# Kernel tuning notes

Measured on AMD Instinct MI355X. Metric: run time of the kernel, lower is better.

## Reference

```python
import jax, jax.numpy as jnp
import numpy as np

B, T, D_MODEL = 2, 2048, 2048
N_HEAD, N_KV = 16, 4
HEAD_DIM = D_MODEL // N_HEAD  # 128
N_REP = N_HEAD // N_KV        # 4
ROPE_BASE = 10000.0


def setup_inputs() -> dict:
    key = jax.random.key(0)
    ks = jax.random.split(key, 5)
    s = 0.02
    return {
        "x": jax.random.normal(ks[0], (B, T, D_MODEL), dtype=jnp.float32),
        "Wq": jax.random.normal(ks[1], (D_MODEL, N_HEAD * HEAD_DIM), dtype=jnp.float32) * s,
        "Wk": jax.random.normal(ks[2], (D_MODEL, N_KV * HEAD_DIM), dtype=jnp.float32) * s,
        "Wv": jax.random.normal(ks[3], (D_MODEL, N_KV * HEAD_DIM), dtype=jnp.float32) * s,
        "Wo": jax.random.normal(ks[4], (D_MODEL, D_MODEL), dtype=jnp.float32) * s,
    }


def _rope_cos_sin(seq_len, dim, dtype):
    inv_freq = 1.0 / (ROPE_BASE ** (jnp.arange(0, dim, 2, dtype=jnp.float32) / dim))
    t = jnp.arange(seq_len, dtype=jnp.float32)
    freqs = t[:, None] * inv_freq[None, :]          # (T, dim/2)
    emb = jnp.concatenate([freqs, freqs], axis=-1)  # (T, dim)
    return jnp.cos(emb).astype(dtype), jnp.sin(emb).astype(dtype)


def _rotate_half(x):
    half = x.shape[-1] // 2
    return jnp.concatenate([-x[..., half:], x[..., :half]], axis=-1)


def reference(x, Wq, Wk, Wv, Wo):
    Bx, Tx, _ = x.shape
    # projections (weights stored (in, out); equals torch Linear with W^T)
    q = (x @ Wq).reshape(Bx, Tx, N_HEAD, HEAD_DIM).transpose(0, 2, 1, 3)  # (B,H,T,d)
    k = (x @ Wk).reshape(Bx, Tx, N_KV, HEAD_DIM).transpose(0, 2, 1, 3)    # (B,Hkv,T,d)
    v = (x @ Wv).reshape(Bx, Tx, N_KV, HEAD_DIM).transpose(0, 2, 1, 3)

    cos, sin = _rope_cos_sin(Tx, HEAD_DIM, x.dtype)  # (T, d)
    q = q * cos + _rotate_half(q) * sin
    k = k * cos + _rotate_half(k) * sin

    # grouped attention: q grouped by kv head, avoids materializing repeated K/V
    qg = q.reshape(Bx, N_KV, N_REP, Tx, HEAD_DIM)
    scale = 1.0 / np.sqrt(HEAD_DIM)
    att = jnp.einsum('bgrtd,bgsd->bgrts', qg, k) * scale  # (B,Hkv,rep,T,S)
    causal = jnp.tril(jnp.ones((Tx, Tx), dtype=bool))
    att = jnp.where(causal, att, -jnp.inf)
    att = jax.nn.softmax(att, axis=-1)
    y = jnp.einsum('bgrts,bgsd->bgrtd', att, v)           # (B,Hkv,rep,T,d)
    y = y.reshape(Bx, N_HEAD, Tx, HEAD_DIM).transpose(0, 2, 1, 3).reshape(Bx, Tx, D_MODEL)
    return y @ Wo
```

## Files before the change

### kernel.cpp

```cpp
#include <hip/hip_runtime.h>
#include <hip/hip_bf16.h>

typedef unsigned short u16;
typedef unsigned int u32;
typedef __attribute__((ext_vector_type(4))) float f32x4;
typedef __attribute__((ext_vector_type(8))) __bf16 bf16x8;

#define B_   2
#define T_   2048
#define DM   2048
#define NH   16
#define NKV  4
#define HD   128

__device__ __forceinline__ u16 f2bf(float f){
    u32 u = __builtin_bit_cast(u32, f);
    u += 0x7FFFu + ((u >> 16) & 1u);
    return (u16)(u >> 16);
}

__device__ __forceinline__ float ex2(float x){
    float r; asm("v_exp_f32 %0, %1" : "=v"(r) : "v"(x)); return r;
}

__device__ __forceinline__ void gld_lds16(const void* g, void* l){
    __builtin_amdgcn_global_load_lds(
        (const __attribute__((address_space(1))) void*)g,
        (__attribute__((address_space(3))) void*)l, 16, 0, 0);
}

__global__ void cast_v4(const float* __restrict__ in, u16* __restrict__ out){
    int i = blockIdx.x * 256 + threadIdx.x;
    float4 v = ((const float4*)in)[i];
    ushort4 o;
    o.x = f2bf(v.x); o.y = f2bf(v.y); o.z = f2bf(v.z); o.w = f2bf(v.w);
    ((ushort4*)out)[i] = o;
}

__global__ void transAll(const float* __restrict__ Wq, const float* __restrict__ Wk,
                         const float* __restrict__ Wv, const float* __restrict__ Wo,
                         u16* __restrict__ Wqkv, u16* __restrict__ Wot){
    __shared__ float tile[32][33];
    int bx = blockIdx.x;
    const float* W; u16* Out; int N; int nb; int perm;
    if (bx < 64)      { W = Wq; Out = Wqkv;                  N = 2048; nb = bx;      perm = 1; }
    else if (bx < 80) { W = Wk; Out = Wqkv + 2048ull * 2048; N = 512;  nb = bx - 64; perm = 1; }
    else if (bx < 96) { W = Wv; Out = Wqkv + 2560ull * 2048; N = 512;  nb = bx - 80; perm = 0; }
    else              { W = Wo; Out = Wot;                   N = 2048; nb = bx - 96; perm = 0; }
    int n0 = nb * 32, k0 = blockIdx.y * 32;
    int tx = threadIdx.x, ty = threadIdx.y;
#pragma unroll
    for (int i = 0; i < 4; i++)
        tile[ty + i * 8][tx] = W[(size_t)(k0 + ty + i * 8) * N + n0 + tx];
    __syncthreads();
#pragma unroll
    for (int i = 0; i < 4; i++){
        int n = n0 + ty + i * 8;
        int np = perm ? ((n & ~127) | ((n & 63) << 1) | ((n >> 6) & 1)) : n;
        Out[(size_t)np * 2048 + k0 + tx] = f2bf(tile[tx][ty + i * 8]);
    }
}

__global__ void rope_tab(float2* __restrict__ tab){
    int idx = blockIdx.x * 256 + threadIdx.x;
    int i = idx & 63, t = idx >> 6;
    float ang = (float)t * exp2f((float)i * (-13.287712379549449f / 64.0f));
    float sv, cv;
    __sincosf(ang, &sv, &cv);
    tab[idx] = make_float2(cv, sv);
}

#define BARR() { __builtin_amdgcn_s_barrier(); __builtin_amdgcn_sched_barrier(0); }
#define LGKM0() { asm volatile("s_waitcnt lgkmcnt(0)" ::: "memory"); __builtin_amdgcn_sched_barrier(0); }
#define VM4() { asm volatile("s_waitcnt vmcnt(4)" ::: "memory"); __builtin_amdgcn_sched_barrier(0); }

#define READ_A(QA, BUF) { \
    const char* ab = (const char*)&As[BUF][wm][0]; \
    _Pragma("unroll") for (int i = 0; i < 4; i++){ \
        int rh = ((QA)*4 + i)*16 + lx; \
        _Pragma("unroll") for (int ks = 0; ks < 2; ks++) \
            a_[i][ks] = *(const bf16x8*)(ab + rh*128 + (((ks*4+tg)*16) ^ ((lx&7)<<4))); \
    } }
#define READ_B(QB, BUF) { \
    const char* bb = (const char*)&Bs[BUF][wn>>1][0]; \
    _Pragma("unroll") for (int n = 0; n < 2; n++){ \
        int rbh = (wn&1)*64 + ((QB)*2+n)*16 + lx; \
        _Pragma("unroll") for (int ks = 0; ks < 2; ks++) \
            b_[(QB)*2+n][ks] = *(const bf16x8*)(bb + rbh*128 + (((ks*4+tg)*16) ^ ((lx&7)<<4))); \
    } }
#define MFMA_Q(QA, QB) { \
    __builtin_amdgcn_s_setprio(1); \
    _Pragma("unroll") for (int i = 0; i < 4; i++) \
    _Pragma("unroll") for (int n = 0; n < 2; n++) \
    _Pragma("unroll") for (int ks = 0; ks < 2; ks++) \
        acc[(QA)*4+i][(QB)*2+n] = __builtin_amdgcn_mfma_f32_16x16x32_bf16( \
            a_[i][ks], b_[(QB)*2+n][ks], acc[(QA)*4+i][(QB)*2+n], 0, 0, 0); \
    __builtin_amdgcn_s_setprio(0); }

template<int MODE>
__global__ __launch_bounds__(512, 2) void gemm256(const u16* __restrict__ A, const u16* __restrict__ Bt,
                                                  void* __restrict__ O0, u16* __restrict__ Ktl,
                                                  u16* __restrict__ Vtl, const float2* __restrict__ tab,
                                                  int NBX){
    __shared__ __attribute__((aligned(16))) u16 As[2][2][8192];
    __shared__ __attribute__((aligned(16))) u16 Bs[2][2][8192];
    const int tid = threadIdx.x;
    const int lane = tid & 63, w = tid >> 6;
    const int wm = w >> 2, wn = w & 3;
    const int tg = lane >> 4, lx = lane & 15;
    int q8 = (int)gridDim.x >> 3;
    int swz = ((int)blockIdx.x & 7) * q8 + ((int)blockIdx.x >> 3);
    const int bx = swz % NBX, by = swz / NBX;
    const int m0 = by * 256, n0 = bx * 256;
    const int K = 2048;
    const int kcx = (lane & 7) ^ ((lane >> 3) & 7);

    f32x4 acc[8][4];
    const f32x4 Z = {0.f, 0.f, 0.f, 0.f};
#pragma unroll
    for (int i = 0; i < 8; i++)
#pragma unroll
        for (int j = 0; j < 4; j++) acc[i][j] = Z;
    bf16x8 a_[4][2], b_[4][2];

    auto stA = [&](int buf, int q, int kt){
        int mh = w >> 2;
        int s0 = (w & 3) * 2;
#pragma unroll
        for (int l = 0; l < 2; l++){
            int s = s0 + l;
            gld_lds16(A + (size_t)(m0 + mh*128 + q*64 + s*8 + (lane>>3)) * K + kt*64 + kcx*8,
                      &As[buf][mh][q*4096 + s*512 + lane*8]);
        }
    };
    auto stB = [&](int buf, int q, int kt){
        int bh = w >> 2;
        int hi = (w >> 1) & 1;
        int s0 = (w & 1) * 2;
#pragma unroll
        for (int l = 0; l < 2; l++){
            int s = s0 + l;
            gld_lds16(Bt + (size_t)(n0 + bh*128 + hi*64 + q*32 + s*8 + (lane>>3)) * K + kt*64 + kcx*8,
                      &Bs[buf][bh][hi*4096 + q*2048 + s*512 + lane*8]);
        }
    };

    stA(0, 0, 0); stB(0, 0, 0); stA(0, 1, 0); stB(0, 1, 0);
    stA(1, 0, 1); stB(1, 0, 1);
    VM4(); BARR();

#pragma unroll 1
    for (int it = 0; it < 16; it++){
        const int T1 = 2*it + 1;
        const int T2 = (2*it + 2 < 32) ? 2*it + 2 : 31;
        const int T3 = (2*it + 3 < 32) ? 2*it + 3 : 31;
        READ_A(0, 0); READ_B(0, 0); stA(1, 1, T1);
        BARR(); LGKM0(); MFMA_Q(0, 0); BARR();
        READ_B(1, 0); stB(1, 1, T1);
        BARR(); LGKM0(); MFMA_Q(0, 1); BARR();
        READ_A(1, 0); stA(0, 0, T2);
        BARR(); LGKM0(); MFMA_Q(1, 0); BARR();
        stB(0, 0, T2);
        BARR(); MFMA_Q(1, 1); VM4(); BARR();
        READ_A(0, 1); READ_B(0, 1); stA(0, 1, T2);
        BARR(); LGKM0(); MFMA_Q(0, 0); BARR();
        READ_B(1, 1); stB(0, 1, T2);
        BARR(); LGKM0(); MFMA_Q(0, 1); BARR();
        READ_A(1, 1); stA(1, 0, T3);
        BARR(); LGKM0(); MFMA_Q(1, 0); BARR();
        stB(1, 0, T3);
        BARR(); MFMA_Q(1, 1); VM4(); BARR();
    }

    if constexpr (MODE == 0){
        float* C = (float*)O0;
#pragma unroll
        for (int mi = 0; mi < 8; mi++)
#pragma unroll
            for (int ni = 0; ni < 4; ni++){
                int r0 = m0 + wm*128 + mi*16 + tg*4;
                int c  = n0 + wn*64 + ni*16 + lx;
#pragma unroll
                for (int j = 0; j < 4; j++)
                    C[(size_t)(r0 + j) * 2048 + c] = acc[mi][ni][j];
            }
    } else {
        u16* Qp = (u16*)O0;
        if (bx < 8){
            const float QS = 0.08838834764831845f * 1.4426950408889634f;
#pragma unroll
            for (int mi = 0; mi < 8; mi++)
#pragma unroll
                for (int ni = 0; ni < 4; ni++){
                    int r0 = m0 + wm*128 + mi*16 + tg*4;
                    int c  = n0 + wn*64 + ni*16 + lx;
                    int ii = (c & 127) >> 1;
#pragma unroll
                    for (int j = 0; j < 4; j++){
                        float v = acc[mi][ni][j];
                        float p = __shfl_xor(v, 1);
                        int t = (r0 + j) & 2047;
                        float2 cs = tab[t * 64 + ii];
                        float o = ((lx & 1) ? (v * cs.x + p * cs.y) : (v * cs.x - p * cs.y)) * QS;
                        Qp[(size_t)(r0 + j) * 2048 + c] = f2bf(o);
                    }
                }
        } else if (bx < 10){
#pragma unroll
            for (int mi = 0; mi < 8; mi++)
#pragma unroll
                for (int ni = 0; ni < 4; ni++){
                    int r0 = m0 + wm*128 + mi*16 + tg*4;
                    int c  = n0 + wn*64 + ni*16 + lx;
                    int hk = (c >> 7) & 3;
                    int dd = c & 127;
                    int ii = dd >> 1;
#pragma unroll
                    for (int j = 0; j < 4; j++){
                        int r = r0 + j;
                        int bb2 = r >> 11, tt = r & 2047;
                        float v = acc[mi][ni][j];
                        float p = __shfl_xor(v, 1);
                        float2 cs = tab[tt * 64 + ii];
                        float o = (lx & 1) ? (v * cs.x + p * cs.y) : (v * cs.x - p * cs.y);
                        size_t tb = ((size_t)(bb2 * 4 + hk) * 32 + (tt >> 6)) * 8192;
                        u32 byte = (u32)((tt & 63) * 256) + (((u32)(2 * dd)) ^ ((u32)((tt & 7) << 4)));
                        Ktl[tb + byte / 2] = f2bf(o);
                    }
                }
        } else {
#pragma unroll
            for (int mi = 0; mi < 8; mi++){
                int r0 = m0 + wm*128 + mi*16 + tg*4;
                int bb2 = r0 >> 11, ss = r0 & 2047;
                int sb = ss & 63;
#pragma unroll
                for (int ni = 0; ni < 4; ni++){
                    int c  = n0 + wn*64 + ni*16 + lx;
                    int hk = (c >> 7) & 3;
                    int d  = c & 127;
                    size_t tb = ((size_t)(bb2 * 4 + hk) * 32 + (ss >> 6)) * 8192;
                    u32 swzd = (u32)((d & 7) << 4);
#pragma unroll
                    for (int j = 0; j < 4; j++){
                        int s = sb + j;
                        int sig = ((s & 15) << 2) | ((s >> 4) & 3);
                        u32 byte = (u32)(d * 128) + (((u32)(2 * sig)) ^ swzd);
                        Vtl[tb + byte / 2] = f2bf(acc[mi][ni][j]);
                    }
                }
            }
        }
    }
}

__global__ __launch_bounds__(256) void attn5(const u16* __restrict__ Q, const u16* __restrict__ Kt,
                                             const u16* __restrict__ Vt, u16* __restrict__ Y){
    __shared__ __attribute__((aligned(16))) u16 Ks[2][64 * 128];
    __shared__ __attribute__((aligned(16))) u16 Vs[2][64 * 128];
    __shared__ __attribute__((aligned(16))) u16 Pl[4][16 * 64];
    const int lane = threadIdx.x & 63, w = threadIdx.x >> 6;
    const int jb = blockIdx.x, h = blockIdx.y, b = blockIdx.z;
    const int hkv = h >> 2;
    const size_t kvBase = ((size_t)(b * NKV + hkv) * 32) * 8192;
    const f32x4 Z = {0.f, 0.f, 0.f, 0.f};
    const int tg = lane >> 4, lx = lane & 15;

    auto STAGE = [&](int buf, int it){
        const u16* kg = Kt + kvBase + (size_t)it * 8192;
        const u16* vg = Vt + kvBase + (size_t)it * 8192;
#pragma unroll
        for (int i = 0; i < 4; i++){
            int is = w * 4 + i;
            gld_lds16(kg + is * 512 + lane * 8, &Ks[buf][is * 512]);
            gld_lds16(vg + is * 512 + lane * 8, &Vs[buf][is * 512]);
        }
    };

#pragma unroll 1
    for (int pass = 0; pass < 2; pass++){
        const int qt = pass == 0 ? jb : 31 - jb;
        const int q0 = qt * 64;
        const int qrow = q0 + w * 16 + lx;
        bf16x8 qfr[4];
#pragma unroll
        for (int kk = 0; kk < 4; kk++)
            qfr[kk] = *(const bf16x8*)(Q + (size_t)(b * T_ + qrow) * DM + h * HD + kk * 32 + tg * 8);
        f32x4 accO[8];
#pragma unroll
        for (int i = 0; i < 8; i++) accO[i] = Z;
        float mr[4] = {-INFINITY, -INFINITY, -INFINITY, -INFINITY};
        float lp[4] = {0.f, 0.f, 0.f, 0.f};
        const int nIter = qt + 1;

        STAGE(0, 0);
        __syncthreads();
        int cur = 0;

#pragma unroll 1
        for (int it = 0; it < nIter; it++){
            if (it + 1 < nIter) STAGE(cur ^ 1, it + 1);
            f32x4 sa[4];
#pragma unroll
            for (int c = 0; c < 4; c++) sa[c] = Z;
            __builtin_amdgcn_s_setprio(1);
#pragma unroll
            for (int c = 0; c < 4; c++){
                int s = c * 16 + lx;
                u32 swz = (u32)((s & 7) << 4);
                const char* kb = (const char*)&Ks[cur][0] + s * 256;
#pragma unroll
                for (int kk = 0; kk < 4; kk++){
                    bf16x8 kf = *(const bf16x8*)(kb + (((u32)(kk * 64 + tg * 16)) ^ swz));
                    sa[c] = __builtin_amdgcn_mfma_f32_16x16x32_bf16(qfr[kk], kf, sa[c], 0, 0, 0);
                }
            }
            __builtin_amdgcn_s_setprio(0);
            const bool diag = (it == nIter - 1);
            float tl[4];
#pragma unroll
            for (int j = 0; j < 4; j++){
                float a0 = sa[0][j], a1 = sa[1][j], a2 = sa[2][j], a3 = sa[3][j];
                if (diag){
                    int qloc = w * 16 + tg * 4 + j;
                    if (lx      > qloc) a0 = -INFINITY;
                    if (lx + 16 > qloc) a1 = -INFINITY;
                    if (lx + 32 > qloc) a2 = -INFINITY;
                    if (lx + 48 > qloc) a3 = -INFINITY;
                }
                sa[0][j] = a0; sa[1][j] = a1; sa[2][j] = a2; sa[3][j] = a3;
                tl[j] = fmaxf(fmaxf(a0, a1), fmaxf(a2, a3));
            }
            int lok = (tl[0] <= mr[0] + 8.f) && (tl[1] <= mr[1] + 8.f) &&
                      (tl[2] <= mr[2] + 8.f) && (tl[3] <= mr[3] + 8.f);
            if (!__all(lok)){
                float corr[4];
#pragma unroll
                for (int j = 0; j < 4; j++){
                    float t = tl[j];
                    t = fmaxf(t, __shfl_xor(t, 1));
                    t = fmaxf(t, __shfl_xor(t, 2));
                    t = fmaxf(t, __shfl_xor(t, 4));
                    t = fmaxf(t, __shfl_xor(t, 8));
                    float mn = fmaxf(mr[j], t);
                    corr[j] = ex2(mr[j] - mn);
                    mr[j] = mn;
                    lp[j] *= corr[j];
                }
#pragma unroll
                for (int dt = 0; dt < 8; dt++){
                    f32x4 t = accO[dt];
                    t[0] *= corr[0]; t[1] *= corr[1]; t[2] *= corr[2]; t[3] *= corr[3];
                    accO[dt] = t;
                }
            }
#pragma unroll
            for (int j = 0; j < 4; j++){
                float mn = mr[j];
                float p0 = ex2(sa[0][j] - mn), p1 = ex2(sa[1][j] - mn);
                float p2 = ex2(sa[2][j] - mn), p3 = ex2(sa[3][j] - mn);
                lp[j] += p0 + p1 + p2 + p3;
                int rr = tg * 4 + j;
                u32 woff = (u32)(rr * 128) + (((u32)(lx * 8)) ^ ((u32)((rr & 7) << 4)));
                u32 r01, r23;
                asm("v_cvt_pk_bf16_f32 %0, %1, %2" : "=v"(r01) : "v"(p0), "v"(p1));
                asm("v_cvt_pk_bf16_f32 %0, %1, %2" : "=v"(r23) : "v"(p2), "v"(p3));
                uint2 pk2 = make_uint2(r01, r23);
                *(uint2*)((char*)&Pl[w][0] + woff) = pk2;
            }
            bf16x8 pf[2];
            {
                char* pb = (char*)&Pl[w][0] + lx * 128;
                u32 swz = (u32)((lx & 7) << 4);
                pf[0] = *(const bf16x8*)(pb + (((u32)(tg * 16))      ^ swz));
                pf[1] = *(const bf16x8*)(pb + (((u32)(tg * 16 + 64)) ^ swz));
            }
            __builtin_amdgcn_s_setprio(1);
#pragma unroll
            for (int dt = 0; dt < 8; dt++){
                int d = dt * 16 + lx;
                u32 swz = (u32)((d & 7) << 4);
                const char* vb = (const char*)&Vs[cur][0] + d * 128;
                bf16x8 vf0 = *(const bf16x8*)(vb + (((u32)(tg * 16))      ^ swz));
                bf16x8 vf1 = *(const bf16x8*)(vb + (((u32)(tg * 16 + 64)) ^ swz));
                accO[dt] = __builtin_amdgcn_mfma_f32_16x16x32_bf16(pf[0], vf0, accO[dt], 0, 0, 0);
                accO[dt] = __builtin_amdgcn_mfma_f32_16x16x32_bf16(pf[1], vf1, accO[dt], 0, 0, 0);
            }
            __builtin_amdgcn_s_setprio(0);
            __syncthreads();
            cur ^= 1;
        }
        float inv[4];
#pragma unroll
        for (int j = 0; j < 4; j++){
            float s = lp[j];
            s += __shfl_xor(s, 1);
            s += __shfl_xor(s, 2);
            s += __shfl_xor(s, 4);
            s += __shfl_xor(s, 8);
            inv[j] = 1.0f / s;
        }
#pragma unroll
        for (int dt = 0; dt < 8; dt++)
#pragma unroll
            for (int j = 0; j < 4; j++){
                int qr = q0 + w * 16 + tg * 4 + j;
                int d = dt * 16 + lx;
                Y[(size_t)(b * T_ + qr) * DM + h * HD + d] = f2bf(accO[dt][j] * inv[j]);
            }
    }
}

extern "C" void kernel_launch(void* const* d_in, const int* in_sizes, int n_in,
                              void* d_out, int out_size, void* d_ws, size_t ws_size,
                              hipStream_t stream){
    const float* x  = (const float*)d_in[0];
    const float* Wq = (const float*)d_in[1];
    const float* Wk = (const float*)d_in[2];
    const float* Wv = (const float*)d_in[3];
    const float* Wo = (const float*)d_in[4];

    char* ws = (char*)d_ws;
    size_t off = 0;
    auto alloc = [&](size_t bytes){ void* p = ws + off; off += (bytes + 255) & ~255ull; return p; };
    u16*    xb   = (u16*)alloc(4096ull * 2048 * 2);
    u16*    Wqkv = (u16*)alloc(3072ull * 2048 * 2);
    u16*    Wot  = (u16*)alloc(2048ull * 2048 * 2);
    u16*    qbb  = (u16*)alloc(4096ull * 2048 * 2);
    u16*    ktl  = (u16*)alloc(2ull * 4 * 32 * 8192 * 2);
    u16*    vtl  = (u16*)alloc(2ull * 4 * 32 * 8192 * 2);
    u16*    ybb  = (u16*)alloc(4096ull * 2048 * 2);
    float2* tab  = (float2*)alloc(2048ull * 64 * 8);

    cast_v4<<<8192, 256, 0, stream>>>(x, xb);
    transAll<<<dim3(160, 64), dim3(32, 8), 0, stream>>>(Wq, Wk, Wv, Wo, Wqkv, Wot);
    rope_tab<<<512, 256, 0, stream>>>(tab);

    gemm256<1><<<192, 512, 0, stream>>>(xb, Wqkv, qbb, ktl, vtl, tab, 12);

    attn5<<<dim3(16, 16, 2), 256, 0, stream>>>(qbb, ktl, vtl, ybb);

    gemm256<0><<<128, 512, 0, stream>>>(ybb, Wot, d_out, nullptr, nullptr, nullptr, 8);
}
```

Before: 216.2 us.

## Shrink GEMM tile to 128x256 to double block count and restructure pipeline

Replaces the 256x256 GEMM tile with a 128x256 tile, halving the per-block A tile and accumulators. The projection and output GEMMs launch twice as many blocks (384 and 256), so they fill the 256 CUs of the MI355X better than 192 and 128 blocks did. The inner loop is rewritten into four phases, with stage loads interleaved differently. The scheduling barriers after s_barrier and vmcnt waits are also removed. Arithmetic intensity per block drops and there is more global traffic for B. Removing the sched_barriers risks the compiler reordering around the hand-tuned waits.

```diff
diff --git a/kernel.cpp b/kernel.cpp
--- a/kernel.cpp
+++ b/kernel.cpp
@@ -70,40 +70,40 @@
     tab[idx] = make_float2(cv, sv);
 }
 
-#define BARR() { __builtin_amdgcn_s_barrier(); __builtin_amdgcn_sched_barrier(0); }
+#define BARR() __builtin_amdgcn_s_barrier()
 #define LGKM0() { asm volatile("s_waitcnt lgkmcnt(0)" ::: "memory"); __builtin_amdgcn_sched_barrier(0); }
-#define VM4() { asm volatile("s_waitcnt vmcnt(4)" ::: "memory"); __builtin_amdgcn_sched_barrier(0); }
-
-#define READ_A(QA, BUF) { \
-    const char* ab = (const char*)&As[BUF][wm][0]; \
-    _Pragma("unroll") for (int i = 0; i < 4; i++){ \
-        int rh = ((QA)*4 + i)*16 + lx; \
+#define VM4() asm volatile("s_waitcnt vmcnt(4)" ::: "memory")
+
+#define READ_A(BUF) { \
+    const char* ab = (const char*)&As[BUF][0]; \
+    _Pragma("unroll") for (int mi = 0; mi < 4; mi++){ \
+        int ra = wm*64 + mi*16 + lx; \
         _Pragma("unroll") for (int ks = 0; ks < 2; ks++) \
-            a_[i][ks] = *(const bf16x8*)(ab + rh*128 + (((ks*4+tg)*16) ^ ((lx&7)<<4))); \
+            a_[mi][ks] = *(const bf16x8*)(ab + ra*128 + (((ks*4+tg)*16) ^ ((lx&7)<<4))); \
     } }
 #define READ_B(QB, BUF) { \
-    const char* bb = (const char*)&Bs[BUF][wn>>1][0]; \
+    const char* bb = (const char*)&Bs[BUF][0] + (QB)*16384; \
     _Pragma("unroll") for (int n = 0; n < 2; n++){ \
-        int rbh = (wn&1)*64 + ((QB)*2+n)*16 + lx; \
+        int rb = wn*32 + n*16 + lx; \
         _Pragma("unroll") for (int ks = 0; ks < 2; ks++) \
-            b_[(QB)*2+n][ks] = *(const bf16x8*)(bb + rbh*128 + (((ks*4+tg)*16) ^ ((lx&7)<<4))); \
+            b_[n][ks] = *(const bf16x8*)(bb + rb*128 + (((ks*4+tg)*16) ^ ((lx&7)<<4))); \
     } }
-#define MFMA_Q(QA, QB) { \
+#define MFMA_P(QB) { \
     __builtin_amdgcn_s_setprio(1); \
-    _Pragma("unroll") for (int i = 0; i < 4; i++) \
+    _Pragma("unroll") for (int mi = 0; mi < 4; mi++) \
     _Pragma("unroll") for (int n = 0; n < 2; n++) \
     _Pragma("unroll") for (int ks = 0; ks < 2; ks++) \
-        acc[(QA)*4+i][(QB)*2+n] = __builtin_amdgcn_mfma_f32_16x16x32_bf16( \
-            a_[i][ks], b_[(QB)*2+n][ks], acc[(QA)*4+i][(QB)*2+n], 0, 0, 0); \
+        acc[mi][(QB)*2+n] = __builtin_amdgcn_mfma_f32_16x16x32_bf16( \
+            a_[mi][ks], b_[n][ks], acc[mi][(QB)*2+n], 0, 0, 0); \
     __builtin_amdgcn_s_setprio(0); }
 
 template<int MODE>
-__global__ __launch_bounds__(512, 2) void gemm256(const u16* __restrict__ A, const u16* __restrict__ Bt,
+__global__ __launch_bounds__(512, 2) void gemm128(const u16* __restrict__ A, const u16* __restrict__ Bt,
                                                   void* __restrict__ O0, u16* __restrict__ Ktl,
                                                   u16* __restrict__ Vtl, const float2* __restrict__ tab,
                                                   int NBX){
-    __shared__ __attribute__((aligned(16))) u16 As[2][2][8192];
-    __shared__ __attribute__((aligned(16))) u16 Bs[2][2][8192];
+    __shared__ __attribute__((aligned(16))) u16 As[2][8192];
+    __shared__ __attribute__((aligned(16))) u16 Bs[2][16384];
     const int tid = threadIdx.x;
     const int lane = tid & 63, w = tid >> 6;
     const int wm = w >> 2, wn = w & 3;
@@ -111,42 +111,38 @@
     int q8 = (int)gridDim.x >> 3;
     int swz = ((int)blockIdx.x & 7) * q8 + ((int)blockIdx.x >> 3);
     const int bx = swz % NBX, by = swz / NBX;
-    const int m0 = by * 256, n0 = bx * 256;
+    const int m0 = by * 128, n0 = bx * 256;
     const int K = 2048;
     const int kcx = (lane & 7) ^ ((lane >> 3) & 7);
 
-    f32x4 acc[8][4];
+    f32x4 acc[4][4];
     const f32x4 Z = {0.f, 0.f, 0.f, 0.f};
 #pragma unroll
-    for (int i = 0; i < 8; i++)
+    for (int i = 0; i < 4; i++)
 #pragma unroll
         for (int j = 0; j < 4; j++) acc[i][j] = Z;
-    bf16x8 a_[4][2], b_[4][2];
-
-    auto stA = [&](int buf, int q, int kt){
-        int mh = w >> 2;
-        int s0 = (w & 3) * 2;
+    bf16x8 a_[4][2], b_[2][2];
+
+    auto stA = [&](int buf, int kt){
 #pragma unroll
         for (int l = 0; l < 2; l++){
-            int s = s0 + l;
-            gld_lds16(A + (size_t)(m0 + mh*128 + q*64 + s*8 + (lane>>3)) * K + kt*64 + kcx*8,
-                      &As[buf][mh][q*4096 + s*512 + lane*8]);
+            int s = w * 2 + l;
+            gld_lds16(A + (size_t)(m0 + s*8 + (lane>>3)) * K + kt*64 + kcx*8,
+                      &As[buf][s*512 + lane*8]);
         }
     };
     auto stB = [&](int buf, int q, int kt){
-        int bh = w >> 2;
-        int hi = (w >> 1) & 1;
-        int s0 = (w & 1) * 2;
 #pragma unroll
         for (int l = 0; l < 2; l++){
-            int s = s0 + l;
-            gld_lds16(Bt + (size_t)(n0 + bh*128 + hi*64 + q*32 + s*8 + (lane>>3)) * K + kt*64 + kcx*8,
-                      &Bs[buf][bh][hi*4096 + q*2048 + s*512 + lane*8]);
+            int s = w * 2 + l;
+            int rr = s*8 + (lane>>3);
+            gld_lds16(Bt + (size_t)(n0 + (rr>>5)*64 + q*32 + (rr&31)) * K + kt*64 + kcx*8,
+                      &Bs[buf][q*8192 + s*512 + lane*8]);
         }
     };
 
-    stA(0, 0, 0); stB(0, 0, 0); stA(0, 1, 0); stB(0, 1, 0);
-    stA(1, 0, 1); stB(1, 0, 1);
+    stA(0, 0); stB(0, 0, 0); stB(0, 1, 0);
+    stA(1, 1); stB(1, 0, 1);
     VM4(); BARR();
 
 #pragma unroll 1
@@ -154,31 +150,27 @@
         const int T1 = 2*it + 1;
         const int T2 = (2*it + 2 < 32) ? 2*it + 2 : 31;
         const int T3 = (2*it + 3 < 32) ? 2*it + 3 : 31;
-        READ_A(0, 0); READ_B(0, 0); stA(1, 1, T1);
-        BARR(); LGKM0(); MFMA_Q(0, 0); BARR();
-        READ_B(1, 0); stB(1, 1, T1);
-        BARR(); LGKM0(); MFMA_Q(0, 1); BARR();
-        READ_A(1, 0); stA(0, 0, T2);
-        BARR(); LGKM0(); MFMA_Q(1, 0); BARR();
-        stB(0, 0, T2);
-        BARR(); MFMA_Q(1, 1); VM4(); BARR();
-        READ_A(0, 1); READ_B(0, 1); stA(0, 1, T2);
-        BARR(); LGKM0(); MFMA_Q(0, 0); BARR();
-        READ_B(1, 1); stB(0, 1, T2);
-        BARR(); LGKM0(); MFMA_Q(0, 1); BARR();
-        READ_A(1, 1); stA(1, 0, T3);
-        BARR(); LGKM0(); MFMA_Q(1, 0); BARR();
-        stB(1, 0, T3);
-        BARR(); MFMA_Q(1, 1); VM4(); BARR();
+        READ_A(0); READ_B(0, 0);
+        stB(1, 1, T1);
+        BARR(); LGKM0(); MFMA_P(0); BARR();
+        READ_B(1, 0);
+        stA(0, T2); stB(0, 0, T2);
+        BARR(); LGKM0(); MFMA_P(1); VM4(); BARR();
+        READ_A(1); READ_B(0, 1);
+        stB(0, 1, T2);
+        BARR(); LGKM0(); MFMA_P(0); BARR();
+        READ_B(1, 1);
+        stA(1, T3); stB(1, 0, T3);
+        BARR(); LGKM0(); MFMA_P(1); VM4(); BARR();
     }
 
     if constexpr (MODE == 0){
         float* C = (float*)O0;
 #pragma unroll
-        for (int mi = 0; mi < 8; mi++)
+        for (int mi = 0; mi < 4; mi++)
 #pragma unroll
             for (int ni = 0; ni < 4; ni++){
-                int r0 = m0 + wm*128 + mi*16 + tg*4;
+                int r0 = m0 + wm*64 + mi*16 + tg*4;
                 int c  = n0 + wn*64 + ni*16 + lx;
 #pragma unroll
                 for (int j = 0; j < 4; j++)
@@ -189,10 +181,10 @@
         if (bx < 8){
             const float QS = 0.08838834764831845f * 1.4426950408889634f;
 #pragma unroll
-            for (int mi = 0; mi < 8; mi++)
+            for (int mi = 0; mi < 4; mi++)
 #pragma unroll
                 for (int ni = 0; ni < 4; ni++){
-                    int r0 = m0 + wm*128 + mi*16 + tg*4;
+                    int r0 = m0 + wm*64 + mi*16 + tg*4;
                     int c  = n0 + wn*64 + ni*16 + lx;
                     int ii = (c & 127) >> 1;
 #pragma unroll
@@ -207,10 +199,10 @@
                 }
         } else if (bx < 10){
 #pragma unroll
-            for (int mi = 0; mi < 8; mi++)
+            for (int mi = 0; mi < 4; mi++)
 #pragma unroll
                 for (int ni = 0; ni < 4; ni++){
-                    int r0 = m0 + wm*128 + mi*16 + tg*4;
+                    int r0 = m0 + wm*64 + mi*16 + tg*4;
                     int c  = n0 + wn*64 + ni*16 + lx;
                     int hk = (c >> 7) & 3;
                     int dd = c & 127;
@@ -230,8 +222,8 @@
                 }
         } else {
 #pragma unroll
-            for (int mi = 0; mi < 8; mi++){
-                int r0 = m0 + wm*128 + mi*16 + tg*4;
+            for (int mi = 0; mi < 4; mi++){
+                int r0 = m0 + wm*64 + mi*16 + tg*4;
                 int bb2 = r0 >> 11, ss = r0 & 2047;
                 int sb = ss & 63;
 #pragma unroll
@@ -436,9 +428,9 @@
     transAll<<<dim3(160, 64), dim3(32, 8), 0, stream>>>(Wq, Wk, Wv, Wo, Wqkv, Wot);
     rope_tab<<<512, 256, 0, stream>>>(tab);
 
-    gemm256<1><<<192, 512, 0, stream>>>(xb, Wqkv, qbb, ktl, vtl, tab, 12);
+    gemm128<1><<<384, 512, 0, stream>>>(xb, Wqkv, qbb, ktl, vtl, tab, 12);
 
     attn5<<<dim3(16, 16, 2), 256, 0, stream>>>(qbb, ktl, vtl, ybb);
 
-    gemm256<0><<<128, 512, 0, stream>>>(ybb, Wot, d_out, nullptr, nullptr, nullptr, 8);
-}
+    gemm128<0><<<256, 512, 0, stream>>>(ybb, Wot, d_out, nullptr, nullptr, nullptr, 8);
+}
```

Result: slower. 227.3 us (+5.1%).

## Merge prep kernels into one launch and double-buffer GEMM register fragments

Applied to the files above, without the earlier changes.

Folds the x cast, weight transpose/cast and RoPE table kernels into a single prep launch, dispatching each role by block index to cut launch overhead. The GEMM main loop is reworked to ping-pong between two register sets for A and B fragments, so LDS reads for the next quadrant are issued before the current MFMA block. Explicit lgkmcnt waits and sched_barriers are removed in favour of memory-clobber barriers, and the prologue now preloads two full k-tiles. This should overlap LDS reads with MFMA work, at the cost of more registers and reliance on the compiler inserting correct waits.

```diff
diff --git a/kernel.cpp b/kernel.cpp
--- a/kernel.cpp
+++ b/kernel.cpp
@@ -29,72 +29,74 @@
         (__attribute__((address_space(3))) void*)l, 16, 0, 0);
 }
 
-__global__ void cast_v4(const float* __restrict__ in, u16* __restrict__ out){
-    int i = blockIdx.x * 256 + threadIdx.x;
-    float4 v = ((const float4*)in)[i];
-    ushort4 o;
-    o.x = f2bf(v.x); o.y = f2bf(v.y); o.z = f2bf(v.z); o.w = f2bf(v.w);
-    ((ushort4*)out)[i] = o;
-}
-
-__global__ void transAll(const float* __restrict__ Wq, const float* __restrict__ Wk,
-                         const float* __restrict__ Wv, const float* __restrict__ Wo,
-                         u16* __restrict__ Wqkv, u16* __restrict__ Wot){
+__global__ void prep(const float* __restrict__ x,
+                     const float* __restrict__ Wq, const float* __restrict__ Wk,
+                     const float* __restrict__ Wv, const float* __restrict__ Wo,
+                     u16* __restrict__ xb, u16* __restrict__ Wqkv, u16* __restrict__ Wot,
+                     float2* __restrict__ tab){
     __shared__ float tile[32][33];
-    int bx = blockIdx.x;
-    const float* W; u16* Out; int N; int nb; int perm;
-    if (bx < 64)      { W = Wq; Out = Wqkv;                  N = 2048; nb = bx;      perm = 1; }
-    else if (bx < 80) { W = Wk; Out = Wqkv + 2048ull * 2048; N = 512;  nb = bx - 64; perm = 1; }
-    else if (bx < 96) { W = Wv; Out = Wqkv + 2560ull * 2048; N = 512;  nb = bx - 80; perm = 0; }
-    else              { W = Wo; Out = Wot;                   N = 2048; nb = bx - 96; perm = 0; }
-    int n0 = nb * 32, k0 = blockIdx.y * 32;
-    int tx = threadIdx.x, ty = threadIdx.y;
-#pragma unroll
-    for (int i = 0; i < 4; i++)
-        tile[ty + i * 8][tx] = W[(size_t)(k0 + ty + i * 8) * N + n0 + tx];
-    __syncthreads();
-#pragma unroll
-    for (int i = 0; i < 4; i++){
-        int n = n0 + ty + i * 8;
-        int np = perm ? ((n & ~127) | ((n & 63) << 1) | ((n >> 6) & 1)) : n;
-        Out[(size_t)np * 2048 + k0 + tx] = f2bf(tile[tx][ty + i * 8]);
+    int bid = blockIdx.x, tid = threadIdx.x;
+    if (bid < 8192){
+        int i = bid * 256 + tid;
+        float4 v = ((const float4*)x)[i];
+        ushort4 o;
+        o.x = f2bf(v.x); o.y = f2bf(v.y); o.z = f2bf(v.z); o.w = f2bf(v.w);
+        ((ushort4*)xb)[i] = o;
+    } else if (bid < 18432){
+        int tb = bid - 8192;
+        int bx = tb % 160, byy = tb / 160;
+        const float* W; u16* Out; int N; int nb; int perm;
+        if (bx < 64)      { W = Wq; Out = Wqkv;                  N = 2048; nb = bx;      perm = 1; }
+        else if (bx < 80) { W = Wk; Out = Wqkv + 2048ull * 2048; N = 512;  nb = bx - 64; perm = 1; }
+        else if (bx < 96) { W = Wv; Out = Wqkv + 2560ull * 2048; N = 512;  nb = bx - 80; perm = 0; }
+        else              { W = Wo; Out = Wot;                   N = 2048; nb = bx - 96; perm = 0; }
+        int n0 = nb * 32, k0 = byy * 32;
+        int tx = tid & 31, ty = tid >> 5;
+#pragma unroll
+        for (int i = 0; i < 4; i++)
+            tile[ty + i * 8][tx] = W[(size_t)(k0 + ty + i * 8) * N + n0 + tx];
+        __syncthreads();
+#pragma unroll
+        for (int i = 0; i < 4; i++){
+            int n = n0 + ty + i * 8;
+            int np = perm ? ((n & ~127) | ((n & 63) << 1) | ((n >> 6) & 1)) : n;
+            Out[(size_t)np * 2048 + k0 + tx] = f2bf(tile[tx][ty + i * 8]);
+        }
+    } else {
+        int idx = (bid - 18432) * 256 + tid;
+        int i = idx & 63, t = idx >> 6;
+        float ang = (float)t * exp2f((float)i * (-13.287712379549449f / 64.0f));
+        float sv, cv;
+        __sincosf(ang, &sv, &cv);
+        tab[idx] = make_float2(cv, sv);
     }
 }
 
-__global__ void rope_tab(float2* __restrict__ tab){
-    int idx = blockIdx.x * 256 + threadIdx.x;
-    int i = idx & 63, t = idx >> 6;
-    float ang = (float)t * exp2f((float)i * (-13.287712379549449f / 64.0f));
-    float sv, cv;
-    __sincosf(ang, &sv, &cv);
-    tab[idx] = make_float2(cv, sv);
-}
-
-#define BARR() { __builtin_amdgcn_s_barrier(); __builtin_amdgcn_sched_barrier(0); }
-#define LGKM0() { asm volatile("s_waitcnt lgkmcnt(0)" ::: "memory"); __builtin_amdgcn_sched_barrier(0); }
-#define VM4() { asm volatile("s_waitcnt vmcnt(4)" ::: "memory"); __builtin_amdgcn_sched_barrier(0); }
-
-#define READ_A(QA, BUF) { \
+#define BARM() asm volatile("s_barrier" ::: "memory")
+#define VM4()  asm volatile("s_waitcnt vmcnt(4)" ::: "memory")
+#define VM8()  asm volatile("s_waitcnt vmcnt(8)" ::: "memory")
+
+#define RD_A(SET, QA, BUF) { \
     const char* ab = (const char*)&As[BUF][wm][0]; \
     _Pragma("unroll") for (int i = 0; i < 4; i++){ \
         int rh = ((QA)*4 + i)*16 + lx; \
         _Pragma("unroll") for (int ks = 0; ks < 2; ks++) \
-            a_[i][ks] = *(const bf16x8*)(ab + rh*128 + (((ks*4+tg)*16) ^ ((lx&7)<<4))); \
+            SET[i][ks] = *(const bf16x8*)(ab + rh*128 + (((ks*4+tg)*16) ^ ((lx&7)<<4))); \
     } }
-#define READ_B(QB, BUF) { \
+#define RD_B(SET, QB, BUF) { \
     const char* bb = (const char*)&Bs[BUF][wn>>1][0]; \
     _Pragma("unroll") for (int n = 0; n < 2; n++){ \
         int rbh = (wn&1)*64 + ((QB)*2+n)*16 + lx; \
         _Pragma("unroll") for (int ks = 0; ks < 2; ks++) \
-            b_[(QB)*2+n][ks] = *(const bf16x8*)(bb + rbh*128 + (((ks*4+tg)*16) ^ ((lx&7)<<4))); \
+            SET[n][ks] = *(const bf16x8*)(bb + rbh*128 + (((ks*4+tg)*16) ^ ((lx&7)<<4))); \
     } }
-#define MFMA_Q(QA, QB) { \
+#define MM(ASET, QA, BSET, QB) { \
     __builtin_amdgcn_s_setprio(1); \
     _Pragma("unroll") for (int i = 0; i < 4; i++) \
     _Pragma("unroll") for (int n = 0; n < 2; n++) \
     _Pragma("unroll") for (int ks = 0; ks < 2; ks++) \
         acc[(QA)*4+i][(QB)*2+n] = __builtin_amdgcn_mfma_f32_16x16x32_bf16( \
-            a_[i][ks], b_[(QB)*2+n][ks], acc[(QA)*4+i][(QB)*2+n], 0, 0, 0); \
+            ASET[i][ks], BSET[n][ks], acc[(QA)*4+i][(QB)*2+n], 0, 0, 0); \
     __builtin_amdgcn_s_setprio(0); }
 
 template<int MODE>
@@ -121,7 +123,7 @@
     for (int i = 0; i < 8; i++)
 #pragma unroll
         for (int j = 0; j < 4; j++) acc[i][j] = Z;
-    bf16x8 a_[4][2], b_[4][2];
+    bf16x8 A0[4][2], A1[4][2], B0[2][2], B1[2][2];
 
     auto stA = [&](int buf, int q, int kt){
         int mh = w >> 2;
@@ -145,31 +147,35 @@
         }
     };
 
-    stA(0, 0, 0); stB(0, 0, 0); stA(0, 1, 0); stB(0, 1, 0);
-    stA(1, 0, 1); stB(1, 0, 1);
-    VM4(); BARR();
+    stA(0, 0, 0); stB(0, 0, 0); stB(0, 1, 0); stA(0, 1, 0);
+    stA(1, 0, 1); stB(1, 0, 1); stB(1, 1, 1); stA(1, 1, 1);
+    VM8(); BARM();
+    RD_A(A0, 0, 0); RD_B(B0, 0, 0);
 
 #pragma unroll 1
     for (int it = 0; it < 16; it++){
-        const int T1 = 2*it + 1;
         const int T2 = (2*it + 2 < 32) ? 2*it + 2 : 31;
         const int T3 = (2*it + 3 < 32) ? 2*it + 3 : 31;
-        READ_A(0, 0); READ_B(0, 0); stA(1, 1, T1);
-        BARR(); LGKM0(); MFMA_Q(0, 0); BARR();
-        READ_B(1, 0); stB(1, 1, T1);
-        BARR(); LGKM0(); MFMA_Q(0, 1); BARR();
-        READ_A(1, 0); stA(0, 0, T2);
-        BARR(); LGKM0(); MFMA_Q(1, 0); BARR();
+        RD_B(B1, 1, 0);
+        BARM(); MM(A0, 0, B0, 0); BARM();
+        RD_A(A1, 1, 0);
+        stA(0, 0, T2);
+        BARM(); MM(A0, 0, B1, 1); BARM();
         stB(0, 0, T2);
-        BARR(); MFMA_Q(1, 1); VM4(); BARR();
-        READ_A(0, 1); READ_B(0, 1); stA(0, 1, T2);
-        BARR(); LGKM0(); MFMA_Q(0, 0); BARR();
-        READ_B(1, 1); stB(0, 1, T2);
-        BARR(); LGKM0(); MFMA_Q(0, 1); BARR();
-        READ_A(1, 1); stA(1, 0, T3);
-        BARR(); LGKM0(); MFMA_Q(1, 0); BARR();
+        BARM(); MM(A1, 1, B0, 0); VM4(); BARM();
+        RD_A(A0, 0, 1); RD_B(B0, 0, 1);
+        stA(0, 1, T2); stB(0, 1, T2);
+        BARM(); MM(A1, 1, B1, 1); BARM();
+        RD_B(B1, 1, 1);
+        BARM(); MM(A0, 0, B0, 0); BARM();
+        RD_A(A1, 1, 1);
+        stA(1, 0, T3);
+        BARM(); MM(A0, 0, B1, 1); BARM();
         stB(1, 0, T3);
-        BARR(); MFMA_Q(1, 1); VM4(); BARR();
+        BARM(); MM(A1, 1, B0, 0); VM4(); BARM();
+        RD_A(A0, 0, 0); RD_B(B0, 0, 0);
+        stB(1, 1, T3); stA(1, 1, T3);
+        BARM(); MM(A1, 1, B1, 1); BARM();
     }
 
     if constexpr (MODE == 0){
@@ -432,9 +438,7 @@
     u16*    ybb  = (u16*)alloc(4096ull * 2048 * 2);
     float2* tab  = (float2*)alloc(2048ull * 64 * 8);
 
-    cast_v4<<<8192, 256, 0, stream>>>(x, xb);
-    transAll<<<dim3(160, 64), dim3(32, 8), 0, stream>>>(Wq, Wk, Wv, Wo, Wqkv, Wot);
-    rope_tab<<<512, 256, 0, stream>>>(tab);
+    prep<<<18944, 256, 0, stream>>>(x, Wq, Wk, Wv, Wo, xb, Wqkv, Wot, tab);
 
     gemm256<1><<<192, 512, 0, stream>>>(xb, Wqkv, qbb, ktl, vtl, tab, 12);
 
```

Result: no change. 218.4 us (+1.0%).

## Split-K the output projection GEMM, fuse prep kernels, drop explicit LDS waits

Applied to the files above, without the earlier changes.

Three changes. The Wo projection GEMM now splits K in two across 256 workgroups instead of 128, so every CU has work. Each half writes bf16 partials, and a new reduce kernel sums them into the fp32 output. The three preprocessing kernels (x cast, weight transpose, RoPE table) are merged into one launch. The GEMM pipeline also drops its explicit lgkmcnt waits and sched_barriers and relies on compiler-inserted waits. The cost is extra global traffic for the partials, an additional launch, and bf16 rounding of the partial sums, which lowers output precision.

```diff
diff --git a/kernel.cpp b/kernel.cpp
--- a/kernel.cpp
+++ b/kernel.cpp
@@ -18,6 +18,9 @@
     u += 0x7FFFu + ((u >> 16) & 1u);
     return (u16)(u >> 16);
 }
+__device__ __forceinline__ float bf2f(u16 v){
+    return __builtin_bit_cast(float, (u32)v << 16);
+}
 
 __device__ __forceinline__ float ex2(float x){
     float r; asm("v_exp_f32 %0, %1" : "=v"(r) : "v"(x)); return r;
@@ -29,50 +32,52 @@
         (__attribute__((address_space(3))) void*)l, 16, 0, 0);
 }
 
-__global__ void cast_v4(const float* __restrict__ in, u16* __restrict__ out){
-    int i = blockIdx.x * 256 + threadIdx.x;
-    float4 v = ((const float4*)in)[i];
-    ushort4 o;
-    o.x = f2bf(v.x); o.y = f2bf(v.y); o.z = f2bf(v.z); o.w = f2bf(v.w);
-    ((ushort4*)out)[i] = o;
-}
-
-__global__ void transAll(const float* __restrict__ Wq, const float* __restrict__ Wk,
-                         const float* __restrict__ Wv, const float* __restrict__ Wo,
-                         u16* __restrict__ Wqkv, u16* __restrict__ Wot){
+__global__ void prep(const float* __restrict__ x,
+                     const float* __restrict__ Wq, const float* __restrict__ Wk,
+                     const float* __restrict__ Wv, const float* __restrict__ Wo,
+                     u16* __restrict__ xb, u16* __restrict__ Wqkv, u16* __restrict__ Wot,
+                     float2* __restrict__ tab){
     __shared__ float tile[32][33];
-    int bx = blockIdx.x;
-    const float* W; u16* Out; int N; int nb; int perm;
-    if (bx < 64)      { W = Wq; Out = Wqkv;                  N = 2048; nb = bx;      perm = 1; }
-    else if (bx < 80) { W = Wk; Out = Wqkv + 2048ull * 2048; N = 512;  nb = bx - 64; perm = 1; }
-    else if (bx < 96) { W = Wv; Out = Wqkv + 2560ull * 2048; N = 512;  nb = bx - 80; perm = 0; }
-    else              { W = Wo; Out = Wot;                   N = 2048; nb = bx - 96; perm = 0; }
-    int n0 = nb * 32, k0 = blockIdx.y * 32;
-    int tx = threadIdx.x, ty = threadIdx.y;
-#pragma unroll
-    for (int i = 0; i < 4; i++)
-        tile[ty + i * 8][tx] = W[(size_t)(k0 + ty + i * 8) * N + n0 + tx];
-    __syncthreads();
-#pragma unroll
-    for (int i = 0; i < 4; i++){
-        int n = n0 + ty + i * 8;
-        int np = perm ? ((n & ~127) | ((n & 63) << 1) | ((n >> 6) & 1)) : n;
-        Out[(size_t)np * 2048 + k0 + tx] = f2bf(tile[tx][ty + i * 8]);
+    int bid = blockIdx.x, tid = threadIdx.x;
+    if (bid < 8192){
+        int i = bid * 256 + tid;
+        float4 v = ((const float4*)x)[i];
+        ushort4 o;
+        o.x = f2bf(v.x); o.y = f2bf(v.y); o.z = f2bf(v.z); o.w = f2bf(v.w);
+        ((ushort4*)xb)[i] = o;
+    } else if (bid < 18432){
+        int tb = bid - 8192;
+        int bx = tb % 160, byy = tb / 160;
+        const float* W; u16* Out; int N; int nb; int perm;
+        if (bx < 64)      { W = Wq; Out = Wqkv;                  N = 2048; nb = bx;      perm = 1; }
+        else if (bx < 80) { W = Wk; Out = Wqkv + 2048ull * 2048; N = 512;  nb = bx - 64; perm = 1; }
+        else if (bx < 96) { W = Wv; Out = Wqkv + 2560ull * 2048; N = 512;  nb = bx - 80; perm = 0; }
+        else              { W = Wo; Out = Wot;                   N = 2048; nb = bx - 96; perm = 0; }
+        int n0 = nb * 32, k0 = byy * 32;
+        int tx = tid & 31, ty = tid >> 5;
+#pragma unroll
+        for (int i = 0; i < 4; i++)
+            tile[ty + i * 8][tx] = W[(size_t)(k0 + ty + i * 8) * N + n0 + tx];
+        __syncthreads();
+#pragma unroll
+        for (int i = 0; i < 4; i++){
+            int n = n0 + ty + i * 8;
+            int np = perm ? ((n & ~127) | ((n & 63) << 1) | ((n >> 6) & 1)) : n;
+            Out[(size_t)np * 2048 + k0 + tx] = f2bf(tile[tx][ty + i * 8]);
+        }
+    } else {
+        int idx = (bid - 18432) * 256 + tid;
+        int i = idx & 63, t = idx >> 6;
+        float ang = (float)t * exp2f((float)i * (-13.287712379549449f / 64.0f));
+        float sv, cv;
+        __sincosf(ang, &sv, &cv);
+        tab[idx] = make_float2(cv, sv);
     }
 }
 
-__global__ void rope_tab(float2* __restrict__ tab){
-    int idx = blockIdx.x * 256 + threadIdx.x;
-    int i = idx & 63, t = idx >> 6;
-    float ang = (float)t * exp2f((float)i * (-13.287712379549449f / 64.0f));
-    float sv, cv;
-    __sincosf(ang, &sv, &cv);
-    tab[idx] = make_float2(cv, sv);
-}
-
-#define BARR() { __builtin_amdgcn_s_barrier(); __builtin_amdgcn_sched_barrier(0); }
-#define LGKM0() { asm volatile("s_waitcnt lgkmcnt(0)" ::: "memory"); __builtin_amdgcn_sched_barrier(0); }
-#define VM4() { asm volatile("s_waitcnt vmcnt(4)" ::: "memory"); __builtin_amdgcn_sched_barrier(0); }
+#define BARR() asm volatile("s_barrier" ::: "memory")
+#define VM4()  asm volatile("s_waitcnt vmcnt(4)" ::: "memory")
+#define VM8()  asm volatile("s_waitcnt vmcnt(8)" ::: "memory")
 
 #define READ_A(QA, BUF) { \
     const char* ab = (const char*)&As[BUF][wm][0]; \
@@ -110,9 +115,14 @@
     const int tg = lane >> 4, lx = lane & 15;
     int q8 = (int)gridDim.x >> 3;
     int swz = ((int)blockIdx.x & 7) * q8 + ((int)blockIdx.x >> 3);
+    int kh = 0;
+    if constexpr (MODE == 2){ kh = swz >> 7; swz &= 127; }
     const int bx = swz % NBX, by = swz / NBX;
     const int m0 = by * 256, n0 = bx * 256;
     const int K = 2048;
+    const int NIT = (MODE == 2) ? 8 : 16;
+    const int kt0 = kh * 16;
+    const int ltMax = 2 * NIT - 1;
     const int kcx = (lane & 7) ^ ((lane >> 3) & 7);
 
     f32x4 acc[8][4];
@@ -145,35 +155,35 @@
         }
     };
 
-    stA(0, 0, 0); stB(0, 0, 0); stA(0, 1, 0); stB(0, 1, 0);
-    stA(1, 0, 1); stB(1, 0, 1);
+    stA(0, 0, kt0); stB(0, 0, kt0); stA(0, 1, kt0); stB(0, 1, kt0);
+    stA(1, 0, kt0 + 1); stB(1, 0, kt0 + 1);
     VM4(); BARR();
 
 #pragma unroll 1
-    for (int it = 0; it < 16; it++){
-        const int T1 = 2*it + 1;
-        const int T2 = (2*it + 2 < 32) ? 2*it + 2 : 31;
-        const int T3 = (2*it + 3 < 32) ? 2*it + 3 : 31;
+    for (int it = 0; it < NIT; it++){
+        const int T1 = kt0 + 2*it + 1;
+        const int T2 = kt0 + ((2*it + 2 < ltMax) ? 2*it + 2 : ltMax);
+        const int T3 = kt0 + ((2*it + 3 < ltMax) ? 2*it + 3 : ltMax);
         READ_A(0, 0); READ_B(0, 0); stA(1, 1, T1);
-        BARR(); LGKM0(); MFMA_Q(0, 0); BARR();
+        BARR(); MFMA_Q(0, 0); BARR();
         READ_B(1, 0); stB(1, 1, T1);
-        BARR(); LGKM0(); MFMA_Q(0, 1); BARR();
+        BARR(); MFMA_Q(0, 1); BARR();
         READ_A(1, 0); stA(0, 0, T2);
-        BARR(); LGKM0(); MFMA_Q(1, 0); BARR();
+        BARR(); MFMA_Q(1, 0); BARR();
         stB(0, 0, T2);
         BARR(); MFMA_Q(1, 1); VM4(); BARR();
         READ_A(0, 1); READ_B(0, 1); stA(0, 1, T2);
-        BARR(); LGKM0(); MFMA_Q(0, 0); BARR();
+        BARR(); MFMA_Q(0, 0); BARR();
         READ_B(1, 1); stB(0, 1, T2);
-        BARR(); LGKM0(); MFMA_Q(0, 1); BARR();
+        BARR(); MFMA_Q(0, 1); BARR();
         READ_A(1, 1); stA(1, 0, T3);
-        BARR(); LGKM0(); MFMA_Q(1, 0); BARR();
+        BARR(); MFMA_Q(1, 0); BARR();
         stB(1, 0, T3);
         BARR(); MFMA_Q(1, 1); VM4(); BARR();
     }
 
-    if constexpr (MODE == 0){
-        float* C = (float*)O0;
+    if constexpr (MODE == 2){
+        u16* C = (u16*)O0 + (size_t)kh * 4096 * 2048;
 #pragma unroll
         for (int mi = 0; mi < 8; mi++)
 #pragma unroll
@@ -182,7 +192,7 @@
                 int c  = n0 + wn*64 + ni*16 + lx;
 #pragma unroll
                 for (int j = 0; j < 4; j++)
-                    C[(size_t)(r0 + j) * 2048 + c] = acc[mi][ni][j];
+                    C[(size_t)(r0 + j) * 2048 + c] = f2bf(acc[mi][ni][j]);
             }
     } else {
         u16* Qp = (u16*)O0;
@@ -252,6 +262,23 @@
             }
         }
     }
+}
+
+__global__ void reduceWo(const u16* __restrict__ P, float* __restrict__ out){
+    size_t t = (size_t)blockIdx.x * 256 + threadIdx.x;
+    const u16* p0 = P + t * 8;
+    const u16* p1 = P + 4096ull * 2048 + t * 8;
+    uint4 a = *(const uint4*)p0;
+    uint4 b = *(const uint4*)p1;
+    const u16* as = (const u16*)&a;
+    const u16* bs = (const u16*)&b;
+    float4 o0, o1;
+    o0.x = bf2f(as[0]) + bf2f(bs[0]); o0.y = bf2f(as[1]) + bf2f(bs[1]);
+    o0.z = bf2f(as[2]) + bf2f(bs[2]); o0.w = bf2f(as[3]) + bf2f(bs[3]);
+    o1.x = bf2f(as[4]) + bf2f(bs[4]); o1.y = bf2f(as[5]) + bf2f(bs[5]);
+    o1.z = bf2f(as[6]) + bf2f(bs[6]); o1.w = bf2f(as[7]) + bf2f(bs[7]);
+    ((float4*)out)[t * 2]     = o0;
+    ((float4*)out)[t * 2 + 1] = o1;
 }
 
 __global__ __launch_bounds__(256) void attn5(const u16* __restrict__ Q, const u16* __restrict__ Kt,
@@ -430,15 +457,15 @@
     u16*    ktl  = (u16*)alloc(2ull * 4 * 32 * 8192 * 2);
     u16*    vtl  = (u16*)alloc(2ull * 4 * 32 * 8192 * 2);
     u16*    ybb  = (u16*)alloc(4096ull * 2048 * 2);
+    u16*    pbb  = (u16*)alloc(2ull * 4096 * 2048 * 2);
     float2* tab  = (float2*)alloc(2048ull * 64 * 8);
 
-    cast_v4<<<8192, 256, 0, stream>>>(x, xb);
-    transAll<<<dim3(160, 64), dim3(32, 8), 0, stream>>>(Wq, Wk, Wv, Wo, Wqkv, Wot);
-    rope_tab<<<512, 256, 0, stream>>>(tab);
+    prep<<<18944, 256, 0, stream>>>(x, Wq, Wk, Wv, Wo, xb, Wqkv, Wot, tab);
 
     gemm256<1><<<192, 512, 0, stream>>>(xb, Wqkv, qbb, ktl, vtl, tab, 12);
 
     attn5<<<dim3(16, 16, 2), 256, 0, stream>>>(qbb, ktl, vtl, ybb);
 
-    gemm256<0><<<128, 512, 0, stream>>>(ybb, Wot, d_out, nullptr, nullptr, nullptr, 8);
-}
+    gemm256<2><<<256, 512, 0, stream>>>(ybb, Wot, pbb, nullptr, nullptr, nullptr, 8);
+    reduceWo<<<4096, 256, 0, stream>>>(pbb, (float*)d_out);
+}
```

Result: faster. 203.5 us (-5.9%).
